# Optimization experiments

Hardware: AMD Instinct MI355X
Metric: run time of the kernel (lower is better)

The kernel has to match this reference:

```python
import jax, jax.numpy as jnp
import numpy as np

B, N, E_PER = 2048, 64, 512            # graphs, nodes/graph, edges/graph
D_NODE, D_EMB = 16, 64                 # env.node_state_dim, node_embedding_size
D_USER, D_UEMB = 32, 64                # env.user_state_dim, user_embedding_size
HID = 512
TOTAL_N, TOTAL_E = B * N, B * E_PER


def setup_inputs() -> dict:
    key = jax.random.key(0)
    ks = jax.random.split(key, 16)
    off = (jnp.arange(B, dtype=jnp.int32) * N)[:, None]
    src = jax.random.randint(ks[0], (B, E_PER), 0, N, dtype=jnp.int32) + off
    dst = jax.random.randint(ks[1], (B, E_PER), 0, N, dtype=jnp.int32) + off
    edge_index = jnp.stack([src.reshape(-1), dst.reshape(-1)])  # [2, TOTAL_E]
    s = lambda k, shape, sc=0.05: jax.random.normal(k, shape, jnp.float32) * sc
    return {
        "x": jax.random.normal(ks[2], (TOTAL_N, D_NODE), jnp.float32),
        "edge_attr": jax.random.normal(ks[3], (TOTAL_E, 2), jnp.float32),
        "user_s": jax.random.normal(ks[4], (B, D_USER), jnp.float32),
        "W_msg": s(ks[5], (D_NODE, D_EMB)), "b_msg": jnp.zeros((D_EMB,), jnp.float32),
        "W_edge": s(ks[6], (2, D_EMB)),     "b_edge": jnp.zeros((D_EMB,), jnp.float32),
        "W_self": s(ks[7], (D_NODE, D_EMB)),"b_self": jnp.zeros((D_EMB,), jnp.float32),
        "W1": s(ks[8], (D_USER, D_UEMB)),   "b1": jnp.zeros((D_UEMB,), jnp.float32),
        "W2": s(ks[9], (N * D_EMB + D_UEMB, HID)), "b2": jnp.zeros((HID,), jnp.float32),
        "W3": s(ks[10], (HID, HID // 2)),   "b3": jnp.zeros((HID // 2,), jnp.float32),
        "W4": s(ks[11], (HID // 2, N), 0.01), "b4": jnp.zeros((N,), jnp.float32),
        "edge_index": edge_index,
    }


def reference(x, edge_attr, user_s, W_msg, b_msg, W_edge, b_edge, W_self, b_self,
              W1, b1, W2, b2, W3, b3, W4, b4, edge_index):
    src, dst = edge_index[0], edge_index[1]
    # GeneralConv (PyG): msg = lin_msg(x_j) + lin_edge(e); sum-aggregate at dst; + lin_self(x_i)
    msg = x[src] @ W_msg + b_msg + edge_attr @ W_edge + b_edge          # [TOTAL_E, D_EMB]
    agg = jax.ops.segment_sum(msg, dst, num_segments=TOTAL_N)          # [TOTAL_N, D_EMB]
    node = jax.nn.relu(agg + x @ W_self + b_self)
    # F.dropout(p=0.5, training=True) -- deterministic mask for the reference
    keep = jax.random.bernoulli(jax.random.key(42), 0.5, node.shape)
    node = jnp.where(keep, node * 2.0, 0.0)
    user = jax.nn.relu(user_s @ W1 + b1)                               # [B, D_UEMB]
    states = jnp.concatenate([node.reshape(B, N * D_EMB), user], axis=1)
    h = jax.nn.relu(states @ W2 + b2)
    h = jax.nn.relu(h @ W3 + b3)
    logits = h @ W4 + b4                                               # [B, N]
    # torch: unsqueeze(dim=0) then softmax(dim=1) => softmax across the BATCH axis
    return jax.nn.softmax(logits, axis=0)[None]                        # [1, B, N]
```

## Files before the change

kernel.cpp:

```cpp
#include <hip/hip_runtime.h>
#include <stdint.h>

#define B_GRAPHS 2048
#define CHUNK 256
#define E_PER 512
#define D_USER 32
#define HID 512
#define GK 4160
#define STATES_DIM 4160
#define WS_FALLBACK 6356992
#define WS_FAST 54067200

typedef unsigned short u16;
typedef unsigned int u32;
typedef __attribute__((ext_vector_type(8))) short short8;
typedef __attribute__((ext_vector_type(4))) float f32x4;

__device__ __forceinline__ float bf2f(u16 b) {
    union { uint32_t u; float f; } c; c.u = ((uint32_t)b) << 16; return c.f;
}
__device__ __forceinline__ u16 f2bf(float f) {
    union { float f; uint32_t u; } c; c.f = f;
    uint32_t u = c.u;
    return (u16)((u + 0x7FFFu + ((u >> 16) & 1u)) >> 16);
}
__device__ __forceinline__ void unpack2(uint32_t w, float& lo, float& hi) {
    union { uint32_t u; float f; } a, b;
    a.u = w << 16; b.u = w & 0xFFFF0000u;
    lo = a.f; hi = b.f;
}

__device__ __forceinline__ void gload16(const u16* g, u16* l) {
    __builtin_amdgcn_global_load_lds(
        (const __attribute__((address_space(1))) void*)g,
        (__attribute__((address_space(3))) void*)l, 16, 0, 0);
}

__device__ __forceinline__ uint32_t rotl32(uint32_t v, int r) {
    return (v << r) | (v >> (32 - r));
}
__device__ __forceinline__ void threefry_0_42(uint32_t x0, uint32_t x1,
                                              uint32_t& o0, uint32_t& o1) {
    const uint32_t ks0 = 0u, ks1 = 42u, ks2 = 0x1BD11BDAu ^ 42u;
    x0 += ks0; x1 += ks1;
#define TFR(r) { x0 += x1; x1 = rotl32(x1, (r)); x1 ^= x0; }
    TFR(13) TFR(15) TFR(26) TFR(6)
    x0 += ks1; x1 += ks2 + 1u;
    TFR(17) TFR(29) TFR(16) TFR(24)
    x0 += ks2; x1 += ks0 + 2u;
    TFR(13) TFR(15) TFR(26) TFR(6)
    x0 += ks0; x1 += ks1 + 3u;
    TFR(17) TFR(29) TFR(16) TFR(24)
    x0 += ks1; x1 += ks2 + 4u;
    TFR(13) TFR(15) TFR(26) TFR(6)
    x0 += ks2; x1 += ks0 + 5u;
#undef TFR
    o0 = x0; o1 = x1;
}
__device__ __forceinline__ bool keep_bit(uint32_t j) {
    uint32_t o0, o1;
    threefry_0_42(0u, j, o0, o1);
    return (((o0 ^ o1) >> 31) == 0u);
}

__global__ __launch_bounds__(256) void fill_kernel(float* __restrict__ out, float v, int n) {
    int i = blockIdx.x * 256 + threadIdx.x;
    if (i < n) out[i] = v;
}

__device__ __forceinline__ void trans32(float (*sT)[33],
                                        const float* __restrict__ W,
                                        u16* __restrict__ WT,
                                        int K, int N, int k0, int n0, int tid) {
    const int tr = tid >> 5, tc = tid & 31;
    #pragma unroll
    for (int i = 0; i < 32; i += 8)
        sT[tr + i][tc] = W[(size_t)(k0 + tr + i) * N + n0 + tc];
    __syncthreads();
    #pragma unroll
    for (int i = 0; i < 32; i += 8)
        WT[(size_t)(n0 + tr + i) * K + k0 + tc] = f2bf(sT[tc][tr + i]);
}

#define SM_SCNT  0
#define SM_SXT   8192
#define SM_SA2   10496
#define SM_WCAT  15616
#define SM_ESUM  20736
#define SM_DEG   21248
#define SM_SIZE  21504

__global__ __launch_bounds__(256) void node_prep(
    const float* __restrict__ x, const float* __restrict__ edge_attr,
    const float* __restrict__ user_s,
    const float* __restrict__ W_msg, const float* __restrict__ W_self,
    const float* __restrict__ b_msg, const float* __restrict__ W_edge,
    const float* __restrict__ b_edge, const float* __restrict__ b_self,
    const float* __restrict__ W1, const float* __restrict__ b1,
    const int* __restrict__ src, const int* __restrict__ dst,
    const float* __restrict__ W2, u16* __restrict__ W2T,
    const float* __restrict__ W3, u16* __restrict__ W3T,
    u16* __restrict__ states)
{
    __shared__ __align__(16) char smem[SM_SIZE];
    const int tid = threadIdx.x;

    if (blockIdx.x >= B_GRAPHS) {
        float (*sT)[33] = (float(*)[33])smem;
        int b = blockIdx.x - B_GRAPHS;
        if (b < 2080) {
            trans32(sT, W2, W2T, 4160, 512, (b % 130) * 32, (b / 130) * 32, tid);
        } else {
            b -= 2080;
            trans32(sT, W3, W3T, 512, 256, (b % 16) * 32, (b / 16) * 32, tid);
        }
        return;
    }

    u32 (*scnt)[32]  = (u32(*)[32])(smem + SM_SCNT);
    u16 (*sxT)[72]   = (u16(*)[72])(smem + SM_SXT);
    u16 (*sA2)[40]   = (u16(*)[40])(smem + SM_SA2);
    u16* sWcat       = (u16*)(smem + SM_WCAT);
    float (*sesum)[64] = (float(*)[64])(smem + SM_ESUM);
    float* sdeg      = (float*)(smem + SM_DEG);

    const int g = blockIdx.x;
    const int w = tid >> 6, lane = tid & 63;
    const int lm = lane & 15, q = lane >> 4;

    const float* xg = x + (size_t)g * 1024;
    const float4 xv = *(const float4*)&xg[tid * 4];
    const int ge0 = g * E_PER + tid, ge1 = ge0 + 256;
    const int s0 = src[ge0] - g * 64, d0 = dst[ge0] - g * 64;
    const int s1 = src[ge1] - g * 64, d1 = dst[ge1] - g * 64;
    const float2* ea2 = (const float2*)edge_attr;
    const float2 a0 = ea2[ge0], a1 = ea2[ge1];
    float bs[4], bm[4], we0[4], we1[4];
    #pragma unroll
    for (int nt = 0; nt < 4; ++nt) {
        int e = nt * 16 + lm;
        bs[nt]  = b_self[e];
        bm[nt]  = b_msg[e] + b_edge[e];
        we0[nt] = W_edge[e];
        we1[nt] = W_edge[64 + e];
    }
    {
        uint4 z = make_uint4(0, 0, 0, 0);
        u32* c0 = &scnt[0][0] + tid * 8;
        *(uint4*)(c0) = z; *(uint4*)(c0 + 4) = z;
    }
    if (tid < 128) ((float*)sesum)[tid] = 0.f;
    u32 kmask = 0;
    #pragma unroll
    for (int r = 0; r < 4; ++r) {
        const uint32_t jb = (uint32_t)g * 4096u
                          + (uint32_t)((16 * w + q * 4 + r) * 64 + lm);
        #pragma unroll
        for (int nt = 0; nt < 4; ++nt)
            if (keep_bit(jb + (uint32_t)(nt * 16))) kmask |= 1u << (r * 4 + nt);
    }
    {
        #pragma unroll
        for (int i = 0; i < 8; ++i) {
            int idx = tid + 256 * i;
            int e = idx >> 5, k = idx & 31;
            float v = (k < 16) ? W_msg[k * 64 + e] : W_self[(k - 16) * 64 + e];
            sWcat[e * 40 + k] = f2bf(v);
        }
    }
    {
        const int n = tid >> 2, kb = (tid & 3) * 4;
        u16 x0 = f2bf(xv.x), x1 = f2bf(xv.y), x2 = f2bf(xv.z), x3 = f2bf(xv.w);
        sxT[kb + 0][n] = x0; sxT[kb + 1][n] = x1;
        sxT[kb + 2][n] = x2; sxT[kb + 3][n] = x3;
        *(ushort4*)&sA2[n][16 + kb] = make_ushort4(x0, x1, x2, x3);
    }
    __syncthreads();

    atomicAdd(&scnt[d0][(s0 >> 1) ^ ((d0 & 7) << 2)], 1u << ((s0 & 1) * 16));
    atomicAdd(&scnt[d1][(s1 >> 1) ^ ((d1 & 7) << 2)], 1u << ((s1 & 1) * 16));
    atomicAdd(&sesum[0][d0], a0.x);
    atomicAdd(&sesum[1][d0], a0.y);
    atomicAdd(&sesum[0][d1], a1.x);
    atomicAdd(&sesum[1][d1], a1.y);
    __syncthreads();

    {
        const int d = tid >> 2, sq = tid & 3;
        uint4 c0 = *(const uint4*)&scnt[d][sq * 8];
        uint4 c1 = *(const uint4*)&scnt[d][sq * 8 + 4];
        u32 cw[8] = {c0.x, c0.y, c0.z, c0.w, c1.x, c1.y, c1.z, c1.w};
        u32 pk[8];
        float degp = 0.f;
        #pragma unroll
        for (int j = 0; j < 8; ++j) {
            u32 lo = cw[j] & 0xFFFFu, hi = cw[j] >> 16;
            degp += (float)(lo + hi);
            pk[j] = (u32)f2bf((float)lo) | ((u32)f2bf((float)hi) << 16);
        }
        *(uint4*)&scnt[d][sq * 8]     = make_uint4(pk[0], pk[1], pk[2], pk[3]);
        *(uint4*)&scnt[d][sq * 8 + 4] = make_uint4(pk[4], pk[5], pk[6], pk[7]);
        degp += __shfl_xor(degp, 1, 64);
        degp += __shfl_xor(degp, 2, 64);
        if (sq == 0) sdeg[d] = degp;
    }

    f32x4 accS;
    #pragma unroll
    for (int r = 0; r < 4; ++r) accS[r] = 0.f;
    {
        const char* crow = (const char*)&scnt[16 * w + lm][0];
        const int sw = (lm & 7) << 4;
        #pragma unroll
        for (int kh = 0; kh < 2; ++kh) {
            short8 a = *(const short8*)(crow + (((kh * 64) + q * 16) ^ sw));
            short8 b = *(const short8*)&sxT[lm][kh * 32 + q * 8];
            accS = __builtin_amdgcn_mfma_f32_16x16x32_bf16(a, b, accS, 0, 0, 0);
        }
    }
    #pragma unroll
    for (int r = 0; r < 4; ++r)
        sA2[16 * w + q * 4 + r][lm] = f2bf(accS[r]);

    f32x4 acc2[4];
    #pragma unroll
    for (int nt = 0; nt < 4; ++nt)
        #pragma unroll
        for (int r = 0; r < 4; ++r) acc2[nt][r] = 0.f;
    short8 a2 = *(const short8*)&sA2[16 * w + lm][q * 8];
    #pragma unroll
    for (int nt = 0; nt < 4; ++nt) {
        short8 b2 = *(const short8*)&sWcat[(nt * 16 + lm) * 40 + q * 8];
        acc2[nt] = __builtin_amdgcn_mfma_f32_16x16x32_bf16(a2, b2, acc2[nt], 0, 0, 0);
    }

    u16* out = states + (size_t)g * STATES_DIM;
    #pragma unroll
    for (int r = 0; r < 4; ++r) {
        int n = 16 * w + q * 4 + r;
        float dg = sdeg[n], e0 = sesum[0][n], e1 = sesum[1][n];
        #pragma unroll
        for (int nt = 0; nt < 4; ++nt) {
            float v = acc2[nt][r] + bs[nt] + dg * bm[nt]
                    + e0 * we0[nt] + e1 * we1[nt];
            v = v > 0.f ? v : 0.f;
            v = ((kmask >> (r * 4 + nt)) & 1u) ? v * 2.0f : 0.0f;
            out[n * 64 + nt * 16 + lm] = f2bf(v);
        }
    }
    if (tid < 64) {
        float v = b1[tid];
        const float* us = user_s + (size_t)g * D_USER;
        #pragma unroll
        for (int k = 0; k < D_USER; ++k) v += us[k] * W1[k * 64 + tid];
        out[4096 + tid] = f2bf(v > 0.f ? v : 0.f);
    }
}

__global__ __launch_bounds__(256) void node_fb(
    int g0,
    const float* __restrict__ x, const float* __restrict__ edge_attr,
    const float* __restrict__ user_s,
    const float* __restrict__ W_msg, const float* __restrict__ b_msg,
    const float* __restrict__ W_edge, const float* __restrict__ b_edge,
    const float* __restrict__ W_self, const float* __restrict__ b_self,
    const float* __restrict__ W1, const float* __restrict__ b1,
    const int* __restrict__ src, const int* __restrict__ dst,
    float* __restrict__ states)
{
    const int g = g0 + blockIdx.x;
    const int tid = threadIdx.x;

    __shared__ float sx[64][16];
    __shared__ float sxsum[64][16];
    __shared__ float sesum[64][2];
    __shared__ float sdeg[64];
    __shared__ float sWmsg[16][64];
    __shared__ float sWself[16][64];
    __shared__ float sWedge[2][64];
    __shared__ float sbias[64];
    __shared__ float sbself[64];

    const float* xg = x + (size_t)g * 1024;
    for (int i = tid; i < 1024; i += 256) {
        sx[i >> 4][i & 15] = xg[i];
        ((float*)sxsum)[i] = 0.f;
        ((float*)sWmsg)[i] = W_msg[i];
        ((float*)sWself)[i] = W_self[i];
    }
    if (tid < 128) ((float*)sWedge)[tid] = W_edge[tid];
    if (tid < 64) {
        sbias[tid] = b_msg[tid] + b_edge[tid];
        sbself[tid] = b_self[tid];
        sdeg[tid] = 0.f;
        sesum[tid][0] = 0.f; sesum[tid][1] = 0.f;
    }
    __syncthreads();

    const float2* ea2 = (const float2*)edge_attr;
    for (int e = tid; e < E_PER; e += 256) {
        int ge = g * E_PER + e;
        int s = src[ge] - g * 64;
        int d = dst[ge] - g * 64;
        float2 a = ea2[ge];
        atomicAdd(&sdeg[d], 1.0f);
        atomicAdd(&sesum[d][0], a.x);
        atomicAdd(&sesum[d][1], a.y);
        #pragma unroll
        for (int k = 0; k < 16; ++k) atomicAdd(&sxsum[d][k], sx[s][k]);
    }
    __syncthreads();

    float* out = states + (size_t)blockIdx.x * STATES_DIM;
    #pragma unroll
    for (int i = 0; i < 16; ++i) {
        int idx = tid + 256 * i;
        int n = idx >> 6, e = idx & 63;
        float v = sbself[e] + sdeg[n] * sbias[e]
                + sesum[n][0] * sWedge[0][e] + sesum[n][1] * sWedge[1][e];
        #pragma unroll
        for (int k = 0; k < 16; ++k)
            v += sxsum[n][k] * sWmsg[k][e] + sx[n][k] * sWself[k][e];
        v = v > 0.f ? v : 0.f;
        v = keep_bit((uint32_t)g * 4096u + (uint32_t)idx) ? v * 2.0f : 0.0f;
        out[idx] = v;
    }
    if (tid < 64) {
        float v = b1[tid];
        const float* us = user_s + (size_t)g * D_USER;
        #pragma unroll
        for (int k = 0; k < D_USER; ++k) v += us[k] * W1[k * 64 + tid];
        out[4096 + tid] = v > 0.f ? v : 0.f;
    }
}

__global__ __launch_bounds__(256) void gemm64(
    const u16* __restrict__ A, const u16* __restrict__ BT,
    float* __restrict__ Cpart, int K, int Ksplit, int N, int ntiles,
    int pstride)
{
    const int cpx = gridDim.x >> 3;
    const int bid = blockIdx.x;
    const int wg  = (bid & 7) * cpx + (bid >> 3);
    const int nt  = wg % ntiles, mt = wg / ntiles;
    const int m0 = mt * 64, n0 = nt * 64;
    const int kb = blockIdx.y * Ksplit;

    __shared__ u16 sA[64][64];
    __shared__ u16 sB[64][64];

    const int tid = threadIdx.x;
    const int wave = tid >> 6, lane = tid & 63;
    const int wm = (wave & 1) * 32, wn = (wave >> 1) * 32;
    const int lm = lane & 15, q = lane >> 4;

    f32x4 acc00, acc01, acc10, acc11;
    #pragma unroll
    for (int r = 0; r < 4; ++r) {
        acc00[r] = 0.f; acc01[r] = 0.f; acc10[r] = 0.f; acc11[r] = 0.f;
    }

    const int srow  = wave * 8 + (lane >> 3);
    const int selem = 8 * ((lane & 7) ^ (lane >> 3));
    const u16* pa0 = &A [(size_t)(m0 + srow) * K + kb + selem];
    const u16* pa1 = &A [(size_t)(m0 + 32 + srow) * K + kb + selem];
    const u16* pb0 = &BT[(size_t)(n0 + srow) * K + kb + selem];
    const u16* pb1 = &BT[(size_t)(n0 + 32 + srow) * K + kb + selem];
    u16* lA0 = (u16*)((char*)&sA[0][0] + wave * 1024);
    u16* lA1 = (u16*)((char*)&sA[0][0] + 4096 + wave * 1024);
    u16* lB0 = (u16*)((char*)&sB[0][0] + wave * 1024);
    u16* lB1 = (u16*)((char*)&sB[0][0] + 4096 + wave * 1024);

    const int sw = (lm & 7) << 4;
    const char* cA  = (const char*)sA + (wm + lm) * 128;
    const char* cA2 = cA + 16 * 128;
    const char* cB  = (const char*)sB + (wn + lm) * 128;
    const char* cB2 = cB + 16 * 128;

    for (int k0 = 0; k0 < Ksplit; k0 += 64) {
        gload16(pa0, lA0); gload16(pa1, lA1);
        gload16(pb0, lB0); gload16(pb1, lB1);
        pa0 += 64; pa1 += 64; pb0 += 64; pb1 += 64;
        __syncthreads();
        #pragma unroll
        for (int kh = 0; kh < 2; ++kh) {
            const int off = (kh * 64 + q * 16) ^ sw;
            short8 a0 = *(const short8*)(cA  + off);
            short8 a1 = *(const short8*)(cA2 + off);
            short8 b0 = *(const short8*)(cB  + off);
            short8 b1 = *(const short8*)(cB2 + off);
            acc00 = __builtin_amdgcn_mfma_f32_16x16x32_bf16(a0, b0, acc00, 0, 0, 0);
            acc01 = __builtin_amdgcn_mfma_f32_16x16x32_bf16(a0, b1, acc01, 0, 0, 0);
            acc10 = __builtin_amdgcn_mfma_f32_16x16x32_bf16(a1, b0, acc10, 0, 0, 0);
            acc11 = __builtin_amdgcn_mfma_f32_16x16x32_bf16(a1, b1, acc11, 0, 0, 0);
        }
        __syncthreads();
    }

    float* Cp = Cpart + (size_t)blockIdx.y * pstride;
    #pragma unroll
    for (int r = 0; r < 4; ++r) {
        int m = m0 + wm + q * 4 + r;
        Cp[(size_t)m * N + n0 + wn + lm]              = acc00[r];
        Cp[(size_t)m * N + n0 + wn + 16 + lm]         = acc01[r];
        Cp[(size_t)(m + 16) * N + n0 + wn + lm]       = acc10[r];
        Cp[(size_t)(m + 16) * N + n0 + wn + 16 + lm]  = acc11[r];
    }
}

__global__ __launch_bounds__(256) void bias_relu_sum(
    const float* __restrict__ parts, int pstride, int nsplit,
    const float* __restrict__ bias, u16* __restrict__ out,
    int Nmask, int total4)
{
    int i = blockIdx.x * 256 + threadIdx.x;
    if (i >= total4) return;
    const int base = i * 4;
    float4 v = *(const float4*)&bias[base & Nmask];
    for (int s = 0; s < nsplit; ++s) {
        float4 p = *(const float4*)&parts[(size_t)s * pstride + base];
        v.x += p.x; v.y += p.y; v.z += p.z; v.w += p.w;
    }
    ushort4 o;
    o.x = f2bf(v.x > 0.f ? v.x : 0.f);
    o.y = f2bf(v.y > 0.f ? v.y : 0.f);
    o.z = f2bf(v.z > 0.f ? v.z : 0.f);
    o.w = f2bf(v.w > 0.f ? v.w : 0.f);
    *(ushort4*)&out[base] = o;
}

template<typename AT, typename CT, bool RELU>
__global__ __launch_bounds__(256) void gemm_any(
    const AT* __restrict__ A, const float* __restrict__ B,
    const float* __restrict__ bias, CT* __restrict__ C,
    int M, int N, int K)
{
    __shared__ float sA[32][72];
    __shared__ float sB[32][64];

    const int tid = threadIdx.x;
    const int tx = tid & 15;
    const int ty = tid >> 4;
    const int m0 = blockIdx.x * 64, n0 = blockIdx.y * 64;

    float acc[4][4] = {};

    for (int k0 = 0; k0 < K; k0 += 32) {
        if constexpr (sizeof(AT) == 4) {
            int r = tid >> 3;
            int c = (tid & 7) * 4;
            #pragma unroll
            for (int rr = 0; rr < 64; rr += 32) {
                float4 v = *(const float4*)&((const float*)A)[(size_t)(m0 + r + rr) * K + k0 + c];
                sA[c + 0][r + rr] = v.x; sA[c + 1][r + rr] = v.y;
                sA[c + 2][r + rr] = v.z; sA[c + 3][r + rr] = v.w;
            }
        } else {
            int m = tid >> 2;
            int c = (tid & 3) * 8;
            uint4 v = *(const uint4*)&((const u16*)A)[(size_t)(m0 + m) * K + k0 + c];
            unpack2(v.x, sA[c + 0][m], sA[c + 1][m]);
            unpack2(v.y, sA[c + 2][m], sA[c + 3][m]);
            unpack2(v.z, sA[c + 4][m], sA[c + 5][m]);
            unpack2(v.w, sA[c + 6][m], sA[c + 7][m]);
        }
        {
            int r = tid >> 3;
            int nc = (tid & 7) * 8;
            float4 v0 = *(const float4*)&B[(size_t)(k0 + r) * N + n0 + nc];
            float4 v1 = *(const float4*)&B[(size_t)(k0 + r) * N + n0 + nc + 4];
            sB[r][nc + 0] = v0.x; sB[r][nc + 1] = v0.y;
            sB[r][nc + 2] = v0.z; sB[r][nc + 3] = v0.w;
            sB[r][nc + 4] = v1.x; sB[r][nc + 5] = v1.y;
            sB[r][nc + 6] = v1.z; sB[r][nc + 7] = v1.w;
        }
        __syncthreads();
        #pragma unroll
        for (int kk = 0; kk < 32; ++kk) {
            float4 av = *(const float4*)&sA[kk][ty * 4];
            float4 bv = *(const float4*)&sB[kk][tx * 4];
            float a_[4] = {av.x, av.y, av.z, av.w};
            float b_[4] = {bv.x, bv.y, bv.z, bv.w};
            #pragma unroll
            for (int i = 0; i < 4; ++i)
                #pragma unroll
                for (int j = 0; j < 4; ++j)
                    acc[i][j] += a_[i] * b_[j];
        }
        __syncthreads();
    }

    #pragma unroll
    for (int i = 0; i < 4; ++i) {
        int m = m0 + ty * 4 + i;
        #pragma unroll
        for (int j = 0; j < 4; ++j) {
            int n = n0 + tx * 4 + j;
            float v = acc[i][j] + bias[n];
            if (RELU) v = v > 0.f ? v : 0.f;
            if constexpr (sizeof(CT) == 2) C[(size_t)m * N + n] = (CT)f2bf(v);
            else                           C[(size_t)m * N + n] = (CT)v;
        }
    }
}

__global__ __launch_bounds__(512) void gemv_softmax(
    const u16* __restrict__ h3, const float* __restrict__ W4,
    const float* __restrict__ b4, float* __restrict__ out)
{
    const int n = blockIdx.x;
    const int tid = threadIdx.x;
    __shared__ float sw4[256];
    __shared__ float sred[8];
    const int wid = tid >> 6, lane = tid & 63;

    if (tid < 256) sw4[tid] = W4[tid * 64 + n];
    __syncthreads();
    const float bn = b4[n];

    float v[4];
    #pragma unroll
    for (int i = 0; i < 4; ++i) {
        const u16* row = h3 + (size_t)(tid + 512 * i) * 256;
        float acc = bn;
        #pragma unroll 4
        for (int k = 0; k < 256; k += 8) {
            uint4 hv = *(const uint4*)&row[k];
            float lo, hi;
            unpack2(hv.x, lo, hi); acc += lo * sw4[k]     + hi * sw4[k + 1];
            unpack2(hv.y, lo, hi); acc += lo * sw4[k + 2] + hi * sw4[k + 3];
            unpack2(hv.z, lo, hi); acc += lo * sw4[k + 4] + hi * sw4[k + 5];
            unpack2(hv.w, lo, hi); acc += lo * sw4[k + 6] + hi * sw4[k + 7];
        }
        v[i] = (acc > -1e30f && acc < 1e30f) ? acc : 0.0f;
    }

    float mx = fmaxf(fmaxf(v[0], v[1]), fmaxf(v[2], v[3]));
    #pragma unroll
    for (int off = 32; off > 0; off >>= 1) mx = fmaxf(mx, __shfl_down(mx, off, 64));
    if (lane == 0) sred[wid] = mx;
    __syncthreads();
    if (tid == 0) {
        float m = sred[0];
        #pragma unroll
        for (int j = 1; j < 8; ++j) m = fmaxf(m, sred[j]);
        sred[0] = m;
    }
    __syncthreads();
    mx = sred[0];
    __syncthreads();

    float sum = 0.f;
    #pragma unroll
    for (int i = 0; i < 4; ++i) { v[i] = expf(v[i] - mx); sum += v[i]; }
    #pragma unroll
    for (int off = 32; off > 0; off >>= 1) sum += __shfl_down(sum, off, 64);
    if (lane == 0) sred[wid] = sum;
    __syncthreads();
    if (tid == 0) {
        float s = 0.f;
        #pragma unroll
        for (int j = 0; j < 8; ++j) s += sred[j];
        sred[0] = s;
    }
    __syncthreads();
    float inv = 1.0f / sred[0];
    #pragma unroll
    for (int i = 0; i < 4; ++i) out[(tid + 512 * i) * 64 + n] = v[i] * inv;
}

__global__ __launch_bounds__(256) void softmax_kernel(
    const float* __restrict__ logits, float* __restrict__ out)
{
    const int n = blockIdx.x;
    const int tid = threadIdx.x;
    __shared__ float sred[4];
    const int wid = tid >> 6, lane = tid & 63;

    float v[8];
    #pragma unroll
    for (int i = 0; i < 8; ++i) {
        float t = logits[(tid + 256 * i) * 64 + n];
        v[i] = (t > -1e30f && t < 1e30f) ? t : 0.0f;
    }

    float mx = -3.4e38f;
    #pragma unroll
    for (int i = 0; i < 8; ++i) mx = fmaxf(mx, v[i]);
    #pragma unroll
    for (int off = 32; off > 0; off >>= 1) mx = fmaxf(mx, __shfl_down(mx, off, 64));
    if (lane == 0) sred[wid] = mx;
    __syncthreads();
    if (tid == 0) sred[0] = fmaxf(fmaxf(sred[0], sred[1]), fmaxf(sred[2], sred[3]));
    __syncthreads();
    mx = sred[0];
    __syncthreads();

    float sum = 0.f;
    #pragma unroll
    for (int i = 0; i < 8; ++i) { v[i] = expf(v[i] - mx); sum += v[i]; }
    #pragma unroll
    for (int off = 32; off > 0; off >>= 1) sum += __shfl_down(sum, off, 64);
    if (lane == 0) sred[wid] = sum;
    __syncthreads();
    if (tid == 0) sred[0] = sred[0] + sred[1] + sred[2] + sred[3];
    __syncthreads();
    float inv = 1.0f / sred[0];
    #pragma unroll
    for (int i = 0; i < 8; ++i) out[(tid + 256 * i) * 64 + n] = v[i] * inv;
}

extern "C" void kernel_launch(void* const* d_in, const int* in_sizes, int n_in,
                              void* d_out, int out_size, void* d_ws, size_t ws_size,
                              hipStream_t stream) {
    if (ws_size < (size_t)WS_FALLBACK || n_in < 18) {
        fill_kernel<<<(out_size + 255) / 256, 256, 0, stream>>>((float*)d_out, 0.25f, out_size);
        return;
    }
    {
        const int expect[18] = {2097152, 2097152, 65536, 1024, 64, 128, 64,
                                1024, 64, 2048, 64, 2129920, 512, 131072, 256,
                                16384, 64, 2097152};
        bool ok = true;
        for (int i = 0; i < 18; ++i) ok = ok && (in_sizes[i] == expect[i]);
        if (!ok || out_size != 131072) {
            fill_kernel<<<(out_size + 255) / 256, 256, 0, stream>>>((float*)d_out, 0.125f, out_size);
            return;
        }
    }

    const float* x         = (const float*)d_in[0];
    const float* edge_attr = (const float*)d_in[1];
    const float* user_s    = (const float*)d_in[2];
    const float* W_msg     = (const float*)d_in[3];
    const float* b_msg     = (const float*)d_in[4];
    const float* W_edge    = (const float*)d_in[5];
    const float* b_edge    = (const float*)d_in[6];
    const float* W_self    = (const float*)d_in[7];
    const float* b_self    = (const float*)d_in[8];
    const float* W1        = (const float*)d_in[9];
    const float* b1        = (const float*)d_in[10];
    const float* W2        = (const float*)d_in[11];
    const float* b2        = (const float*)d_in[12];
    const float* W3        = (const float*)d_in[13];
    const float* b3        = (const float*)d_in[14];
    const float* W4        = (const float*)d_in[15];
    const float* b4        = (const float*)d_in[16];
    const int* edge_index  = (const int*)d_in[17];
    const int* src = edge_index;
    const int* dst = edge_index + B_GRAPHS * E_PER;

    float* logits = (float*)d_out;
    char* ws = (char*)d_ws;

    if (ws_size >= (size_t)WS_FAST) {
        u16*   states = (u16*)ws;
        u16*   W2T    = (u16*)(ws + 17039360);
        float* h2part = (float*)(ws + 21299200);
        u16*   h2     = (u16*)(ws + 42270720);
        u16*   W3T    = (u16*)(ws + 44367872);
        float* h3part = (float*)(ws + 44630016);
        u16*   h3     = (u16*)(ws + 53018624);

        node_prep<<<B_GRAPHS + 2208, 256, 0, stream>>>(
            x, edge_attr, user_s, W_msg, W_self, b_msg, W_edge, b_edge,
            b_self, W1, b1, src, dst, W2, W2T, W3, W3T, states);
        gemm64<<<dim3(256, 5), 256, 0, stream>>>(states, W2T, h2part,
                                                 GK, 832, 512, 8, 1048576);
        bias_relu_sum<<<1024, 256, 0, stream>>>(h2part, 1048576, 5, b2, h2,
                                                511, 262144);
        gemm64<<<dim3(128, 4), 256, 0, stream>>>(h2, W3T, h3part,
                                                 512, 128, 256, 4, 524288);
        bias_relu_sum<<<512, 256, 0, stream>>>(h3part, 524288, 4, b3, h3,
                                               255, 131072);
        gemv_softmax<<<64, 512, 0, stream>>>(h3, W4, b4, logits);
    } else {
        float* states = (float*)ws;
        float* h3     = (float*)ws;
        u16*   h2     = (u16*)(ws + 4259840);

        for (int c = 0; c < B_GRAPHS / CHUNK; ++c) {
            node_fb<<<CHUNK, 256, 0, stream>>>(
                c * CHUNK, x, edge_attr, user_s, W_msg, b_msg, W_edge, b_edge,
                W_self, b_self, W1, b1, src, dst, states);
            gemm_any<float, u16, true><<<dim3(CHUNK / 64, HID / 64), 256, 0, stream>>>(
                states, W2, b2, h2 + (size_t)c * CHUNK * HID, CHUNK, HID, STATES_DIM);
        }
        gemm_any<u16,   float, true ><<<dim3(32, 4), 256, 0, stream>>>(
            h2, W3, b3, h3, B_GRAPHS, HID / 2, HID);
        gemm_any<float, float, false><<<dim3(32, 1), 256, 0, stream>>>(
            h3, W4, b4, logits, B_GRAPHS, 64, HID / 2);
        softmax_kernel<<<64, 256, 0, stream>>>(logits, logits);
    }
}
```

Before: 192.1 us.

## Register-prefetch GEMM tiles with padded LDS, compute dropout mask inline

```diff
diff --git a/kernel.cpp b/kernel.cpp
--- a/kernel.cpp
+++ b/kernel.cpp
@@ -28,12 +28,6 @@
     union { uint32_t u; float f; } a, b;
     a.u = w << 16; b.u = w & 0xFFFF0000u;
     lo = a.f; hi = b.f;
-}
-
-__device__ __forceinline__ void gload16(const u16* g, u16* l) {
-    __builtin_amdgcn_global_load_lds(
-        (const __attribute__((address_space(1))) void*)g,
-        (__attribute__((address_space(3))) void*)l, 16, 0, 0);
 }
 
 __device__ __forceinline__ uint32_t rotl32(uint32_t v, int r) {
@@ -150,15 +144,6 @@
         *(uint4*)(c0) = z; *(uint4*)(c0 + 4) = z;
     }
     if (tid < 128) ((float*)sesum)[tid] = 0.f;
-    u32 kmask = 0;
-    #pragma unroll
-    for (int r = 0; r < 4; ++r) {
-        const uint32_t jb = (uint32_t)g * 4096u
-                          + (uint32_t)((16 * w + q * 4 + r) * 64 + lm);
-        #pragma unroll
-        for (int nt = 0; nt < 4; ++nt)
-            if (keep_bit(jb + (uint32_t)(nt * 16))) kmask |= 1u << (r * 4 + nt);
-    }
     {
         #pragma unroll
         for (int i = 0; i < 8; ++i) {
@@ -239,12 +224,13 @@
     for (int r = 0; r < 4; ++r) {
         int n = 16 * w + q * 4 + r;
         float dg = sdeg[n], e0 = sesum[0][n], e1 = sesum[1][n];
+        uint32_t jbase = (uint32_t)g * 4096u + (uint32_t)(n * 64 + lm);
         #pragma unroll
         for (int nt = 0; nt < 4; ++nt) {
             float v = acc2[nt][r] + bs[nt] + dg * bm[nt]
                     + e0 * we0[nt] + e1 * we1[nt];
             v = v > 0.f ? v : 0.f;
-            v = ((kmask >> (r * 4 + nt)) & 1u) ? v * 2.0f : 0.0f;
+            v = keep_bit(jbase + (uint32_t)(nt * 16)) ? v * 2.0f : 0.0f;
             out[n * 64 + nt * 16 + lm] = f2bf(v);
         }
     }
@@ -346,8 +332,8 @@
     const int m0 = mt * 64, n0 = nt * 64;
     const int kb = blockIdx.y * Ksplit;
 
-    __shared__ u16 sA[64][64];
-    __shared__ u16 sB[64][64];
+    __shared__ u16 sA[64][72];
+    __shared__ u16 sB[64][72];
 
     const int tid = threadIdx.x;
     const int wave = tid >> 6, lane = tid & 63;
@@ -360,41 +346,35 @@
         acc00[r] = 0.f; acc01[r] = 0.f; acc10[r] = 0.f; acc11[r] = 0.f;
     }
 
-    const int srow  = wave * 8 + (lane >> 3);
-    const int selem = 8 * ((lane & 7) ^ (lane >> 3));
-    const u16* pa0 = &A [(size_t)(m0 + srow) * K + kb + selem];
-    const u16* pa1 = &A [(size_t)(m0 + 32 + srow) * K + kb + selem];
-    const u16* pb0 = &BT[(size_t)(n0 + srow) * K + kb + selem];
-    const u16* pb1 = &BT[(size_t)(n0 + 32 + srow) * K + kb + selem];
-    u16* lA0 = (u16*)((char*)&sA[0][0] + wave * 1024);
-    u16* lA1 = (u16*)((char*)&sA[0][0] + 4096 + wave * 1024);
-    u16* lB0 = (u16*)((char*)&sB[0][0] + wave * 1024);
-    u16* lB1 = (u16*)((char*)&sB[0][0] + 4096 + wave * 1024);
-
-    const int sw = (lm & 7) << 4;
-    const char* cA  = (const char*)sA + (wm + lm) * 128;
-    const char* cA2 = cA + 16 * 128;
-    const char* cB  = (const char*)sB + (wn + lm) * 128;
-    const char* cB2 = cB + 16 * 128;
+    const int arow = tid >> 2, aseg = (tid & 3) * 16;
+    const u16* pa = &A [(size_t)(m0 + arow) * K + kb + aseg];
+    const u16* pb = &BT[(size_t)(n0 + arow) * K + kb + aseg];
+    uint4 ra0 = *(const uint4*)pa, ra1 = *(const uint4*)(pa + 8);
+    uint4 rb0 = *(const uint4*)pb, rb1 = *(const uint4*)(pb + 8);
 
     for (int k0 = 0; k0 < Ksplit; k0 += 64) {
-        gload16(pa0, lA0); gload16(pa1, lA1);
-        gload16(pb0, lB0); gload16(pb1, lB1);
-        pa0 += 64; pa1 += 64; pb0 += 64; pb1 += 64;
         __syncthreads();
+        *(uint4*)&sA[arow][aseg]     = ra0;
+        *(uint4*)&sA[arow][aseg + 8] = ra1;
+        *(uint4*)&sB[arow][aseg]     = rb0;
+        *(uint4*)&sB[arow][aseg + 8] = rb1;
+        __syncthreads();
+        if (k0 + 64 < Ksplit) {
+            pa += 64; pb += 64;
+            ra0 = *(const uint4*)pa; ra1 = *(const uint4*)(pa + 8);
+            rb0 = *(const uint4*)pb; rb1 = *(const uint4*)(pb + 8);
+        }
         #pragma unroll
         for (int kh = 0; kh < 2; ++kh) {
-            const int off = (kh * 64 + q * 16) ^ sw;
-            short8 a0 = *(const short8*)(cA  + off);
-            short8 a1 = *(const short8*)(cA2 + off);
-            short8 b0 = *(const short8*)(cB  + off);
-            short8 b1 = *(const short8*)(cB2 + off);
+            short8 a0 = *(const short8*)&sA[wm + lm]     [kh * 32 + q * 8];
+            short8 a1 = *(const short8*)&sA[wm + 16 + lm][kh * 32 + q * 8];
+            short8 b0 = *(const short8*)&sB[wn + lm]     [kh * 32 + q * 8];
+            short8 b1 = *(const short8*)&sB[wn + 16 + lm][kh * 32 + q * 8];
             acc00 = __builtin_amdgcn_mfma_f32_16x16x32_bf16(a0, b0, acc00, 0, 0, 0);
             acc01 = __builtin_amdgcn_mfma_f32_16x16x32_bf16(a0, b1, acc01, 0, 0, 0);
             acc10 = __builtin_amdgcn_mfma_f32_16x16x32_bf16(a1, b0, acc10, 0, 0, 0);
             acc11 = __builtin_amdgcn_mfma_f32_16x16x32_bf16(a1, b1, acc11, 0, 0, 0);
         }
-        __syncthreads();
     }
 
     float* Cp = Cpart + (size_t)blockIdx.y * pstride;
```

New measurement: 194.3 us (median of 2 runs). Within noise of the previous version (+1.2%).
